# Optimization experiments

Measured on AMD Instinct MI355X. Metric: run time of the kernel, lower is better.

The kernel has to match this reference:

```python
import jax, jax.numpy as jnp
import numpy as np

N, IN_F, OUT_F = 8192, 4096, 4096
QMIN, QMAX = -128, 127  # int8 range for bitwidth 8


def setup_inputs() -> dict:
    key = jax.random.key(0)
    k1, k2, k3, k4 = jax.random.split(key, 4)
    x = jax.random.randint(k1, (N, IN_F), QMIN, QMAX + 1, dtype=jnp.int32).astype(jnp.int8)
    weight = jax.random.randint(k2, (OUT_F, IN_F), QMIN, QMAX + 1, dtype=jnp.int32).astype(jnp.int8)
    bias = jax.random.randint(k3, (OUT_F,), -1024, 1024, dtype=jnp.int32)
    weight_scale = jax.random.uniform(k4, (OUT_F,), dtype=jnp.float32, minval=0.001, maxval=0.02)
    input_scale = jnp.asarray([0.05], dtype=jnp.float32)
    output_scale = jnp.asarray([0.1], dtype=jnp.float32)
    output_zero_point = 0
    return {"x": x, "weight": weight, "bias": bias, "weight_scale": weight_scale,
            "input_scale": input_scale, "output_scale": output_scale,
            "output_zero_point": output_zero_point}


def reference(x, weight, bias, weight_scale, input_scale, output_scale, output_zero_point):
    # int32-accumulated GEMM with bias (CPU path of the torch module)
    acc = jnp.matmul(x.astype(jnp.int32), weight.astype(jnp.int32).T) + bias[None, :]  # [N, OUT_F] int32
    # fused dequant/requant epilogue
    scale_factor = (input_scale * weight_scale / output_scale)[None, :]  # [1, OUT_F]
    out = acc.astype(jnp.float32) * scale_factor + output_zero_point
    out = jnp.clip(jnp.round(out), QMIN, QMAX).astype(jnp.int8)
    return out
```

## Files before the change

kernel.cpp:

```cpp
#include <hip/hip_runtime.h>
#include <stdint.h>


#define M_DIM 8192
#define N_DIM 4096
#define K_DIM 4096
#define BM 256
#define BN 256
#define BKB 64
#define NT (K_DIM / BKB)
#define NBLK ((M_DIM / BM) * (N_DIM / BN))
#define ABUF (BM * BKB)
#define BBUF (BN * BKB)

using i32x4 = __attribute__((ext_vector_type(4))) int;

typedef const __attribute__((address_space(1))) uint32_t* gptr_t;
typedef __attribute__((address_space(3))) uint32_t* lptr_t;

__device__ __forceinline__ void gload_lds16(const void* g, void* l) {
    __builtin_amdgcn_global_load_lds((gptr_t)g, (lptr_t)l, 16, 0, 0);
}

__device__ __forceinline__ int pack4(i32x4 v) {
    return (int)(((unsigned)v.x & 0xFFu) | (((unsigned)v.y & 0xFFu) << 8) |
                 (((unsigned)v.z & 0xFFu) << 16) | (((unsigned)v.w) << 24));
}

__global__ void pack_i8_kernel(const int* __restrict__ src, int8_t* __restrict__ dst, int n_elems) {
    int idx = blockIdx.x * blockDim.x + threadIdx.x;
    int stride = gridDim.x * blockDim.x;
    int n16 = n_elems >> 4;
    for (int i = idx; i < n16; i += stride) {
        const i32x4* s = (const i32x4*)(src + (size_t)i * 16);
        i32x4 v0 = s[0], v1 = s[1], v2 = s[2], v3 = s[3];
        i32x4 o;
        o.x = pack4(v0); o.y = pack4(v1); o.z = pack4(v2); o.w = pack4(v3);
        *(i32x4*)(dst + (size_t)i * 16) = o;
    }
}

#define MFMA_I8(a, b, c) __builtin_amdgcn_mfma_i32_16x16x64_i8((a), (b), (c), 0, 0, 0)

#define FRAG_A(P, m) (*(const i32x4*)(Acur + ((wr * 128 + (P) * 64 + (m) * 16 + fr) * 64 + fcol)))
#define FRAG_B(n)    (*(const i32x4*)(Bcur + ((wc * 64 + (n) * 16 + fr) * 64 + fcol)))

#define PHASE0(STAGE_STMTS, TAIL_STMTS)                                           \
  { i32x4 af0 = FRAG_A(0,0), af1 = FRAG_A(0,1), af2 = FRAG_A(0,2), af3 = FRAG_A(0,3); \
    bq0 = FRAG_B(0); bq1 = FRAG_B(1); bq2 = FRAG_B(2); bq3 = FRAG_B(3);           \
    STAGE_STMTS;                                                                  \
    __builtin_amdgcn_s_barrier();                                                 \
    asm volatile("s_waitcnt lgkmcnt(0)" ::: "memory");                            \
    __builtin_amdgcn_sched_barrier(0);                                            \
    __builtin_amdgcn_s_setprio(1);                                                \
    acc[0][0]=MFMA_I8(af0,bq0,acc[0][0]); acc[0][1]=MFMA_I8(af0,bq1,acc[0][1]);   \
    acc[0][2]=MFMA_I8(af0,bq2,acc[0][2]); acc[0][3]=MFMA_I8(af0,bq3,acc[0][3]);   \
    acc[1][0]=MFMA_I8(af1,bq0,acc[1][0]); acc[1][1]=MFMA_I8(af1,bq1,acc[1][1]);   \
    acc[1][2]=MFMA_I8(af1,bq2,acc[1][2]); acc[1][3]=MFMA_I8(af1,bq3,acc[1][3]);   \
    acc[2][0]=MFMA_I8(af2,bq0,acc[2][0]); acc[2][1]=MFMA_I8(af2,bq1,acc[2][1]);   \
    acc[2][2]=MFMA_I8(af2,bq2,acc[2][2]); acc[2][3]=MFMA_I8(af2,bq3,acc[2][3]);   \
    acc[3][0]=MFMA_I8(af3,bq0,acc[3][0]); acc[3][1]=MFMA_I8(af3,bq1,acc[3][1]);   \
    acc[3][2]=MFMA_I8(af3,bq2,acc[3][2]); acc[3][3]=MFMA_I8(af3,bq3,acc[3][3]);   \
    __builtin_amdgcn_s_setprio(0);                                                \
    TAIL_STMTS;                                                                   \
    __builtin_amdgcn_s_barrier(); }

#define PHASE1(STAGE_STMTS, TAIL_STMTS)                                           \
  { i32x4 af0 = FRAG_A(1,0), af1 = FRAG_A(1,1), af2 = FRAG_A(1,2), af3 = FRAG_A(1,3); \
    STAGE_STMTS;                                                                  \
    __builtin_amdgcn_s_barrier();                                                 \
    asm volatile("s_waitcnt lgkmcnt(0)" ::: "memory");                            \
    __builtin_amdgcn_sched_barrier(0);                                            \
    __builtin_amdgcn_s_setprio(1);                                                \
    acc[4][0]=MFMA_I8(af0,bq0,acc[4][0]); acc[4][1]=MFMA_I8(af0,bq1,acc[4][1]);   \
    acc[4][2]=MFMA_I8(af0,bq2,acc[4][2]); acc[4][3]=MFMA_I8(af0,bq3,acc[4][3]);   \
    acc[5][0]=MFMA_I8(af1,bq0,acc[5][0]); acc[5][1]=MFMA_I8(af1,bq1,acc[5][1]);   \
    acc[5][2]=MFMA_I8(af1,bq2,acc[5][2]); acc[5][3]=MFMA_I8(af1,bq3,acc[5][3]);   \
    acc[6][0]=MFMA_I8(af2,bq0,acc[6][0]); acc[6][1]=MFMA_I8(af2,bq1,acc[6][1]);   \
    acc[6][2]=MFMA_I8(af2,bq2,acc[6][2]); acc[6][3]=MFMA_I8(af2,bq3,acc[6][3]);   \
    acc[7][0]=MFMA_I8(af3,bq0,acc[7][0]); acc[7][1]=MFMA_I8(af3,bq1,acc[7][1]);   \
    acc[7][2]=MFMA_I8(af3,bq2,acc[7][2]); acc[7][3]=MFMA_I8(af3,bq3,acc[7][3]);   \
    __builtin_amdgcn_s_setprio(0);                                                \
    TAIL_STMTS;                                                                   \
    __builtin_amdgcn_s_barrier(); }

__global__ __launch_bounds__(512, 2)
void qgemm256_kernel(const int8_t* __restrict__ x8, const int8_t* __restrict__ w8,
                     const int* __restrict__ bias, const float* __restrict__ wscale,
                     const float* __restrict__ iscale, const float* __restrict__ oscale,
                     const int* __restrict__ zp, int* __restrict__ out) {
    extern __shared__ int8_t lds[];
    int8_t* As = lds;
    int8_t* Bs = lds + 3 * ABUF;

    const int tid  = threadIdx.x;
    const int wave = tid >> 6;
    const int lane = tid & 63;

    int b = blockIdx.x;
    int s = (b & 7) * (NBLK >> 3) + (b >> 3);
    const int bcol = (s & 15) * BN;
    const int brow = (s >> 4) * BM;

    const int wr = wave >> 2;
    const int wc = wave & 3;

    const int8_t* Ag = x8 + (size_t)(brow + wave * 32 + (lane >> 2)) * K_DIM + (lane & 3) * 16;
    const int8_t* Bg = w8 + (size_t)(bcol + wave * 32 + (lane >> 2)) * K_DIM + (lane & 3) * 16;
    const int aoff = wave * 2048;
    const int boff = wave * 2048;

    const int fr   = lane & 15;
    const int fcol = (lane >> 4) * 16;

    i32x4 acc[8][4] = {};
    i32x4 bq0, bq1, bq2, bq3;

    #pragma unroll
    for (int t0 = 0; t0 < 2; t0++) {
        int8_t* Ad = As + t0 * ABUF;
        int8_t* Bd = Bs + t0 * BBUF;
        const int8_t* Ak = Ag + (size_t)t0 * BKB;
        const int8_t* Bk = Bg + (size_t)t0 * BKB;
        gload_lds16(Ak,               Ad + aoff);
        gload_lds16(Ak + 16 * K_DIM,  Ad + aoff + 1024);
        gload_lds16(Bk,               Bd + boff);
        gload_lds16(Bk + 16 * K_DIM,  Bd + boff + 1024);
    }
    asm volatile("s_waitcnt vmcnt(4)" ::: "memory");
    __builtin_amdgcn_s_barrier();

    int cur = 0, stg = 2;
    for (int t = 0; t < NT - 2; ++t) {
        const int8_t* Acur = As + cur * ABUF;
        const int8_t* Bcur = Bs + cur * BBUF;
        int8_t* Astg = As + stg * ABUF;
        int8_t* Bstg = Bs + stg * BBUF;
        const int8_t* AgK = Ag + (size_t)(t + 2) * BKB;
        const int8_t* BgK = Bg + (size_t)(t + 2) * BKB;

        PHASE0(
            { gload_lds16(AgK,              Astg + aoff);
              gload_lds16(AgK + 16 * K_DIM, Astg + aoff + 1024); },
            ((void)0))
        PHASE1(
            { gload_lds16(BgK,              Bstg + boff);
              gload_lds16(BgK + 16 * K_DIM, Bstg + boff + 1024); },
            asm volatile("s_waitcnt vmcnt(4)" ::: "memory"))

        cur = (cur == 2) ? 0 : cur + 1;
        stg = (stg == 2) ? 0 : stg + 1;
    }
    {
        const int8_t* Acur = As + cur * ABUF;
        const int8_t* Bcur = Bs + cur * BBUF;
        PHASE0(((void)0), ((void)0))
        PHASE1(((void)0), asm volatile("s_waitcnt vmcnt(0)" ::: "memory"))
        cur = (cur == 2) ? 0 : cur + 1;
    }
    {
        const int8_t* Acur = As + cur * ABUF;
        const int8_t* Bcur = Bs + cur * BBUF;
        PHASE0(((void)0), ((void)0))
        PHASE1(((void)0), ((void)0))
    }

    const float is_v = iscale[0];
    const float os_v = oscale[0];
    const float zpf = (float)zp[0];
    #pragma unroll
    for (int n = 0; n < 4; n++) {
        int col = bcol + wc * 64 + n * 16 + (lane & 15);
        float sf = (is_v * wscale[col]) / os_v;
        int bz = bias[col];
        #pragma unroll
        for (int m = 0; m < 8; m++) {
            int row0 = brow + wr * 128 + m * 16 + (lane >> 4) * 4;
            #pragma unroll
            for (int r = 0; r < 4; r++) {
                float v = (float)(acc[m][n][r] + bz) * sf + zpf;
                v = rintf(v);
                v = fminf(fmaxf(v, -128.0f), 127.0f);
                out[(size_t)(row0 + r) * N_DIM + col] = (int)v;
            }
        }
    }
}

__global__ void qgemm_fallback(const int* __restrict__ x32, const int* __restrict__ w32,
                               const int* __restrict__ bias, const float* __restrict__ wscale,
                               const float* __restrict__ iscale, const float* __restrict__ oscale,
                               const int* __restrict__ zp, int* __restrict__ out) {
    __shared__ int8_t As[128][64];
    __shared__ int8_t Bs[128][64];
    const int tid  = threadIdx.x;
    const int wave = tid >> 6;
    const int lane = tid & 63;
    int b = blockIdx.x;
    int s = (b & 7) * (gridDim.x >> 3) + (b >> 3);
    const int bcol = (s & 31) * 128;
    const int brow = (s >> 5) * 128;
    const int wr = wave >> 1;
    const int wc = wave & 1;
    i32x4 acc[4][4] = {};
    for (int kt = 0; kt < K_DIM; kt += 64) {
        int row = tid >> 1;
        int h = tid & 1;
        const i32x4* sa = (const i32x4*)(x32 + (size_t)(brow + row) * K_DIM + kt + h * 32);
        const i32x4* sb = (const i32x4*)(w32 + (size_t)(bcol + row) * K_DIM + kt + h * 32);
        int pa[8], pb[8];
        #pragma unroll
        for (int j = 0; j < 8; j++) { pa[j] = pack4(sa[j]); pb[j] = pack4(sb[j]); }
        *(i32x4*)&As[row][h * 32]      = *(i32x4*)&pa[0];
        *(i32x4*)&As[row][h * 32 + 16] = *(i32x4*)&pa[4];
        *(i32x4*)&Bs[row][h * 32]      = *(i32x4*)&pb[0];
        *(i32x4*)&Bs[row][h * 32 + 16] = *(i32x4*)&pb[4];
        __syncthreads();
        i32x4 a_frag[4], b_frag[4];
        #pragma unroll
        for (int m = 0; m < 4; m++)
            a_frag[m] = *(const i32x4*)&As[wr * 64 + m * 16 + (lane & 15)][(lane >> 4) * 16];
        #pragma unroll
        for (int n = 0; n < 4; n++)
            b_frag[n] = *(const i32x4*)&Bs[wc * 64 + n * 16 + (lane & 15)][(lane >> 4) * 16];
        #pragma unroll
        for (int m = 0; m < 4; m++)
            #pragma unroll
            for (int n = 0; n < 4; n++)
                acc[m][n] = MFMA_I8(a_frag[m], b_frag[n], acc[m][n]);
        __syncthreads();
    }
    const float is_v = iscale[0];
    const float os_v = oscale[0];
    const float zpf = (float)zp[0];
    #pragma unroll
    for (int n = 0; n < 4; n++) {
        int col = bcol + wc * 64 + n * 16 + (lane & 15);
        float sf = (is_v * wscale[col]) / os_v;
        int bz = bias[col];
        #pragma unroll
        for (int m = 0; m < 4; m++) {
            int row0 = brow + wr * 64 + m * 16 + (lane >> 4) * 4;
            #pragma unroll
            for (int r = 0; r < 4; r++) {
                float v = (float)(acc[m][n][r] + bz) * sf + zpf;
                v = rintf(v);
                v = fminf(fmaxf(v, -128.0f), 127.0f);
                out[(size_t)(row0 + r) * N_DIM + col] = (int)v;
            }
        }
    }
}

extern "C" void kernel_launch(void* const* d_in, const int* in_sizes, int n_in,
                              void* d_out, int out_size, void* d_ws, size_t ws_size,
                              hipStream_t stream) {
    const int*   x32    = (const int*)d_in[0];
    const int*   w32    = (const int*)d_in[1];
    const int*   bias   = (const int*)d_in[2];
    const float* wscale = (const float*)d_in[3];
    const float* iscale = (const float*)d_in[4];
    const float* oscale = (const float*)d_in[5];
    const int*   zp     = (const int*)d_in[6];
    int* out = (int*)d_out;

    const size_t need = (size_t)M_DIM * K_DIM + (size_t)N_DIM * K_DIM;
    const size_t lds_bytes = 3 * (size_t)(ABUF + BBUF);

    if (ws_size >= need) {
        int8_t* x8 = (int8_t*)d_ws;
        int8_t* w8 = x8 + (size_t)M_DIM * K_DIM;
        pack_i8_kernel<<<2048, 256, 0, stream>>>(x32, x8, M_DIM * K_DIM);
        pack_i8_kernel<<<1024, 256, 0, stream>>>(w32, w8, N_DIM * K_DIM);
        (void)hipFuncSetAttribute((const void*)qgemm256_kernel,
                                  hipFuncAttributeMaxDynamicSharedMemorySize,
                                  (int)lds_bytes);
        qgemm256_kernel<<<NBLK, 512, lds_bytes, stream>>>(x8, w8, bias, wscale, iscale, oscale, zp, out);
    } else {
        qgemm_fallback<<<2048, 256, 0, stream>>>(x32, w32, bias, wscale, iscale, oscale, zp, out);
    }
}
```

Measured before the change: 201.4 us.

## Pack int8 operands into MFMA-fragment-ordered panels to simplify LDS reads

The int32-to-int8 pack kernels now write operands in 16-row by 64-K panels, ordered so each lane's 16-byte MFMA fragment is contiguous. The GEMM kernel then loads each whole 1 KB panel straight into LDS, and every fragment read becomes a lane-strided linear access. This is meant to remove LDS bank conflicts and cut address arithmetic in the inner loop. The cost is a strided-gather read pattern in the pack kernels and a tighter coupling between the pack and GEMM layouts.

```diff
diff --git a/kernel.cpp b/kernel.cpp
--- a/kernel.cpp
+++ b/kernel.cpp
@@ -8,7 +8,8 @@
 #define BM 256
 #define BN 256
 #define BKB 64
-#define NT (K_DIM / BKB)
+#define NKT (K_DIM / BKB)
+#define NT NKT
 #define NBLK ((M_DIM / BM) * (N_DIM / BN))
 #define ABUF (BM * BKB)
 #define BBUF (BN * BKB)
@@ -27,23 +28,25 @@
                  (((unsigned)v.z & 0xFFu) << 16) | (((unsigned)v.w) << 24));
 }
 
-__global__ void pack_i8_kernel(const int* __restrict__ src, int8_t* __restrict__ dst, int n_elems) {
-    int idx = blockIdx.x * blockDim.x + threadIdx.x;
-    int stride = gridDim.x * blockDim.x;
-    int n16 = n_elems >> 4;
-    for (int i = idx; i < n16; i += stride) {
-        const i32x4* s = (const i32x4*)(src + (size_t)i * 16);
-        i32x4 v0 = s[0], v1 = s[1], v2 = s[2], v3 = s[3];
-        i32x4 o;
-        o.x = pack4(v0); o.y = pack4(v1); o.z = pack4(v2); o.w = pack4(v3);
-        *(i32x4*)(dst + (size_t)i * 16) = o;
-    }
+__global__ void pack_panels_kernel(const int* __restrict__ src, int8_t* __restrict__ dst,
+                                   int n_blocks) {
+    int gid = blockIdx.x * blockDim.x + threadIdx.x;
+    int blk = gid >> 6;
+    int l = gid & 63;
+    if (blk >= n_blocks) return;
+    int rb = blk >> 6;
+    int kt = blk & (NKT - 1);
+    const i32x4* s4 = (const i32x4*)(src + (size_t)(rb * 16 + (l & 15)) * K_DIM
+                                         + kt * 64 + (l >> 4) * 16);
+    i32x4 o;
+    o.x = pack4(s4[0]); o.y = pack4(s4[1]); o.z = pack4(s4[2]); o.w = pack4(s4[3]);
+    *(i32x4*)(dst + (size_t)blk * 1024 + l * 16) = o;
 }
 
 #define MFMA_I8(a, b, c) __builtin_amdgcn_mfma_i32_16x16x64_i8((a), (b), (c), 0, 0, 0)
 
-#define FRAG_A(P, m) (*(const i32x4*)(Acur + ((wr * 128 + (P) * 64 + (m) * 16 + fr) * 64 + fcol)))
-#define FRAG_B(n)    (*(const i32x4*)(Bcur + ((wc * 64 + (n) * 16 + fr) * 64 + fcol)))
+#define FRAG_A(P, m) (*(const i32x4*)(Acur + ((P) * 4 + (m)) * 1024))
+#define FRAG_B(n)    (*(const i32x4*)(Bcur + (n) * 1024))
 
 #define PHASE0(STAGE_STMTS, TAIL_STMTS)                                           \
   { i32x4 af0 = FRAG_A(0,0), af1 = FRAG_A(0,1), af2 = FRAG_A(0,2), af3 = FRAG_A(0,3); \
@@ -85,7 +88,7 @@
     __builtin_amdgcn_s_barrier(); }
 
 __global__ __launch_bounds__(512, 2)
-void qgemm256_kernel(const int8_t* __restrict__ x8, const int8_t* __restrict__ w8,
+void qgemm256_kernel(const int8_t* __restrict__ xp, const int8_t* __restrict__ wp,
                      const int* __restrict__ bias, const float* __restrict__ wscale,
                      const float* __restrict__ iscale, const float* __restrict__ oscale,
                      const int* __restrict__ zp, int* __restrict__ out) {
@@ -105,13 +108,12 @@
     const int wr = wave >> 2;
     const int wc = wave & 3;
 
-    const int8_t* Ag = x8 + (size_t)(brow + wave * 32 + (lane >> 2)) * K_DIM + (lane & 3) * 16;
-    const int8_t* Bg = w8 + (size_t)(bcol + wave * 32 + (lane >> 2)) * K_DIM + (lane & 3) * 16;
+    const int rb0 = brow >> 4;
+    const int cb0 = bcol >> 4;
+    const int8_t* AgP = xp + ((size_t)(rb0 + wave * 2) * NKT) * 1024 + lane * 16;
+    const int8_t* BgP = wp + ((size_t)(cb0 + wave * 2) * NKT) * 1024 + lane * 16;
+    const size_t substep = (size_t)NKT * 1024;
     const int aoff = wave * 2048;
-    const int boff = wave * 2048;
-
-    const int fr   = lane & 15;
-    const int fcol = (lane >> 4) * 16;
 
     i32x4 acc[8][4] = {};
     i32x4 bq0, bq1, bq2, bq3;
@@ -120,47 +122,44 @@
     for (int t0 = 0; t0 < 2; t0++) {
         int8_t* Ad = As + t0 * ABUF;
         int8_t* Bd = Bs + t0 * BBUF;
-        const int8_t* Ak = Ag + (size_t)t0 * BKB;
-        const int8_t* Bk = Bg + (size_t)t0 * BKB;
-        gload_lds16(Ak,               Ad + aoff);
-        gload_lds16(Ak + 16 * K_DIM,  Ad + aoff + 1024);
-        gload_lds16(Bk,               Bd + boff);
-        gload_lds16(Bk + 16 * K_DIM,  Bd + boff + 1024);
+        gload_lds16(AgP + (size_t)t0 * 1024,           Ad + aoff);
+        gload_lds16(AgP + substep + (size_t)t0 * 1024, Ad + aoff + 1024);
+        gload_lds16(BgP + (size_t)t0 * 1024,           Bd + aoff);
+        gload_lds16(BgP + substep + (size_t)t0 * 1024, Bd + aoff + 1024);
     }
     asm volatile("s_waitcnt vmcnt(4)" ::: "memory");
     __builtin_amdgcn_s_barrier();
 
     int cur = 0, stg = 2;
     for (int t = 0; t < NT - 2; ++t) {
-        const int8_t* Acur = As + cur * ABUF;
-        const int8_t* Bcur = Bs + cur * BBUF;
+        const int8_t* Acur = As + cur * ABUF + wr * 8192 + lane * 16;
+        const int8_t* Bcur = Bs + cur * BBUF + wc * 4096 + lane * 16;
         int8_t* Astg = As + stg * ABUF;
         int8_t* Bstg = Bs + stg * BBUF;
-        const int8_t* AgK = Ag + (size_t)(t + 2) * BKB;
-        const int8_t* BgK = Bg + (size_t)(t + 2) * BKB;
+        const size_t koff = (size_t)(t + 2) * 1024;
 
         PHASE0(
-            { gload_lds16(AgK,              Astg + aoff);
-              gload_lds16(AgK + 16 * K_DIM, Astg + aoff + 1024); },
+            { gload_lds16(AgP + koff,           Astg + aoff);
+              gload_lds16(AgP + substep + koff, Astg + aoff + 1024); },
             ((void)0))
         PHASE1(
-            { gload_lds16(BgK,              Bstg + boff);
-              gload_lds16(BgK + 16 * K_DIM, Bstg + boff + 1024); },
+            { gload_lds16(BgP + koff,           Bstg + aoff);
+              gload_lds16(BgP + substep + koff, Bstg + aoff + 1024); },
             asm volatile("s_waitcnt vmcnt(4)" ::: "memory"))
 
         cur = (cur == 2) ? 0 : cur + 1;
         stg = (stg == 2) ? 0 : stg + 1;
     }
     {
-        const int8_t* Acur = As + cur * ABUF;
-        const int8_t* Bcur = Bs + cur * BBUF;
+        const int8_t* Acur = As + cur * ABUF + wr * 8192 + lane * 16;
+        const int8_t* Bcur = Bs + cur * BBUF + wc * 4096 + lane * 16;
         PHASE0(((void)0), ((void)0))
         PHASE1(((void)0), asm volatile("s_waitcnt vmcnt(0)" ::: "memory"))
         cur = (cur == 2) ? 0 : cur + 1;
     }
     {
-        const int8_t* Acur = As + cur * ABUF;
-        const int8_t* Bcur = Bs + cur * BBUF;
+        const int8_t* Acur = As + cur * ABUF + wr * 8192 + lane * 16;
+        const int8_t* Bcur = Bs + cur * BBUF + wc * 4096 + lane * 16;
         PHASE0(((void)0), ((void)0))
         PHASE1(((void)0), ((void)0))
     }
@@ -268,14 +267,16 @@
     const size_t lds_bytes = 3 * (size_t)(ABUF + BBUF);
 
     if (ws_size >= need) {
-        int8_t* x8 = (int8_t*)d_ws;
-        int8_t* w8 = x8 + (size_t)M_DIM * K_DIM;
-        pack_i8_kernel<<<2048, 256, 0, stream>>>(x32, x8, M_DIM * K_DIM);
-        pack_i8_kernel<<<1024, 256, 0, stream>>>(w32, w8, N_DIM * K_DIM);
+        int8_t* xp = (int8_t*)d_ws;
+        int8_t* wp = xp + (size_t)M_DIM * K_DIM;
+        const int nblkA = (M_DIM / 16) * NKT;
+        const int nblkB = (N_DIM / 16) * NKT;
+        pack_panels_kernel<<<nblkA / 4, 256, 0, stream>>>(x32, xp, nblkA);
+        pack_panels_kernel<<<nblkB / 4, 256, 0, stream>>>(w32, wp, nblkB);
         (void)hipFuncSetAttribute((const void*)qgemm256_kernel,
                                   hipFuncAttributeMaxDynamicSharedMemorySize,
                                   (int)lds_bytes);
-        qgemm256_kernel<<<NBLK, 512, lds_bytes, stream>>>(x8, w8, bias, wscale, iscale, oscale, zp, out);
+        qgemm256_kernel<<<NBLK, 512, lds_bytes, stream>>>(xp, wp, bias, wscale, iscale, oscale, zp, out);
     } else {
         qgemm_fallback<<<2048, 256, 0, stream>>>(x32, w32, bias, wscale, iscale, oscale, zp, out);
     }
```

New measurement: 187.6 us. 6.9% less time.
